# Optimization experiments

Hardware: AMD Instinct MI355X
Metric: run time of the kernel (lower is better)

The kernel has to match this reference:

```python
import jax, jax.numpy as jnp
import numpy as np

D_MODEL, D_STATE, D_CONV, EXPAND, N_HEADS = 768, 64, 4, 2, 12
D_INNER = D_MODEL * EXPAND           # 1536
HEAD_DIM = D_INNER // N_HEADS        # 128
IN_PROJ = D_INNER * 2 + N_HEADS * D_STATE * 2 + N_HEADS  # 4620
EPS = 1e-5


def setup_inputs() -> dict:
    key = jax.random.key(0)
    ks = jax.random.split(key, 8)
    s = lambda fan_in: 1.0 / np.sqrt(fan_in)
    return {
        "x": jax.random.normal(ks[0], (1, 1024, D_MODEL), dtype=jnp.float32),
        "W_in": jax.random.normal(ks[1], (IN_PROJ, D_MODEL), dtype=jnp.float32) * s(D_MODEL),
        "conv_w": jax.random.normal(ks[2], (D_INNER, D_CONV), dtype=jnp.float32) * s(D_CONV),
        "conv_b": jnp.zeros((D_INNER,), dtype=jnp.float32),
        "A_log": jnp.full((N_HEADS,), np.log(0.5), dtype=jnp.float32),
        "Dp": jnp.ones((N_HEADS,), dtype=jnp.float32),
        "dt_bias": jnp.zeros((N_HEADS,), dtype=jnp.float32),
        "W_out": jax.random.normal(ks[3], (D_MODEL, D_INNER), dtype=jnp.float32) * s(D_INNER),
        "norm_w": jnp.ones((D_INNER,), dtype=jnp.float32),
    }


def _causal_conv1d(x, w, b):
    # x: (B,L,Din), depthwise causal conv with kernel size D_CONV
    L = x.shape[1]
    xp = jnp.pad(x, ((0, 0), (D_CONV - 1, 0), (0, 0)))
    y = b
    for i in range(D_CONV):  # fixed small kernel, unrolled
        y = y + xp[:, i:i + L, :] * w[:, i]
    return y


def reference(x, W_in, conv_w, conv_b, A_log, Dp, dt_bias, W_out, norm_w):
    B_sz, L, _ = x.shape
    nh, ds, hd = N_HEADS, D_STATE, HEAD_DIM
    proj = jnp.einsum('bld,pd->blp', x, W_in)
    z = proj[:, :, :D_INNER]
    x_ssm = proj[:, :, D_INNER:2 * D_INNER]
    o = 2 * D_INNER
    Bm = proj[:, :, o:o + nh * ds].reshape(B_sz, L, nh, ds)
    Cm = proj[:, :, o + nh * ds:o + 2 * nh * ds].reshape(B_sz, L, nh, ds)
    dt_r = proj[:, :, o + 2 * nh * ds:]
    dt = jax.nn.softplus(dt_r) + dt_bias[None, None, :]          # (B,L,nh)

    x_ssm = jax.nn.silu(_causal_conv1d(x_ssm, conv_w, conv_b))
    x_ssm = x_ssm.reshape(B_sz, L, nh, hd)

    A = -jnp.exp(A_log)                                          # (nh,)
    log_decay = A[None, None, :] * dt                            # (B,L,nh)
    Phi = jnp.cumsum(log_decay, axis=1)
    dB = dt[..., None] * Bm                                      # (B,L,nh,ds)
    # b: (B,L,nh,hd,ds) outer product
    b = dB[:, :, :, None, :] * x_ssm[..., None]
    max_exp = 80.0
    exp_neg_Phi = jnp.exp(jnp.minimum(-Phi, max_exp))[..., None, None]
    b_cumsum = jnp.cumsum(exp_neg_Phi * b, axis=1)
    h = jnp.exp(Phi)[..., None, None] * b_cumsum                 # (B,L,nh,hd,ds)
    y = jnp.sum(Cm[:, :, :, None, :] * h, axis=-1)               # (B,L,nh,hd)
    y = y + Dp[None, None, :, None] * x_ssm
    y = y.reshape(B_sz, L, D_INNER)

    # RMSNorm then gate
    rms = jax.lax.rsqrt(jnp.mean(y * y, axis=-1, keepdims=True) + EPS)
    y = y * rms * norm_w
    y = y * jax.nn.silu(z)
    return jnp.einsum('bli,di->bld', y, W_out)
```

## Files before the change

kernel.cpp:

```cpp
#include <hip/hip_runtime.h>
#include <cmath>

#define LSEQ   1024
#define NPROJ  4620
#define NPADW  4736
#define DINNER 1536
#define NH     12
#define HDIM   128
#define OFF_Z  0
#define OFF_X  1536
#define OFF_B  3072
#define OFF_C  3840
#define OFF_DT 4608

typedef unsigned short u16;
typedef unsigned int u32;
typedef short bf16x8 __attribute__((ext_vector_type(8)));
typedef float f32x4 __attribute__((ext_vector_type(4)));

__device__ inline u16 f2b(float f) {
  unsigned u = __float_as_uint(f);
  return (u16)((u + 0x7fffu + ((u >> 16) & 1u)) >> 16);
}
__device__ inline float b2f(u16 h) { return __uint_as_float(((unsigned)h) << 16); }
__device__ inline u32 pk2(float a, float b) { return (u32)f2b(a) | ((u32)f2b(b) << 16); }

__device__ inline void gll16(const void* g, void* l) {
  __builtin_amdgcn_global_load_lds((const __attribute__((address_space(1))) void*)g,
                                   (__attribute__((address_space(3))) void*)l, 16, 0, 0);
}

#define S0N 196608
#define S1N 909312
#define S1V 887040
#define S2N 294912
__global__ __launch_bounds__(256) void ksplit_all(const float* __restrict__ x,
    const float* __restrict__ Wi, const float* __restrict__ Wo,
    u16* __restrict__ Ah, u16* __restrict__ Wh, u16* __restrict__ Woh) {
  int i = blockIdx.x * 256 + threadIdx.x;
  const float* src; u16* hi; int j, valid;
  if (i < S0N)            { src = x;  hi = Ah;  j = i;              valid = S0N; }
  else if (i < S0N + S1N) { src = Wi; hi = Wh;  j = i - S0N;        valid = S1V; }
  else                    { src = Wo; hi = Woh; j = i - S0N - S1N;  valid = S2N; }
  float4 v = (j < valid) ? ((const float4*)src)[j] : make_float4(0.f, 0.f, 0.f, 0.f);
  ((uint2*)hi)[j] = make_uint2(pk2(v.x, v.y), pk2(v.z, v.w));
}

template<int BM, int BN, int MAP, bool NG, bool OBF>
__global__ __launch_bounds__(256) void gemm1(const u16* __restrict__ Ah,
    const u16* __restrict__ Wh, void* __restrict__ Cv, float* __restrict__ dtr,
    int lda, int ldw, int Ksl, int Nreal, int ldc) {
  constexpr int PLA = BM * 64;
  constexpr int PB = PLA + BN * 64;
  constexpr int IA = BM / 8, ITOT = IA + BN / 8;
  constexpr int FRn = BN / 32;
  __shared__ u16 lds[2 * PB];
  const int tid = threadIdx.x;
  const int l = tid & 63, w = tid >> 6;
  const int wm = w >> 1, wn = w & 1;
  const int kg = l >> 4, li = l & 15;

  int b = blockIdx.x, m0, n0, koff, cslice = 0;
  if (MAP == 0) {
    int xcd = b & 7, idx = b >> 3;
    m0 = (idx & 15) * 64;
    n0 = (xcd * 5 + (idx >> 4)) * 128;
    koff = 0;
    if (NG && n0 >= NPADW) return;
  } else {
    int xcd = b & 7, idx = b >> 3;
    int gg = xcd * 6 + (idx >> 4);
    m0 = (idx & 15) * 64;
    n0 = (gg % 12) * 64;
    koff = (gg / 12) * 384;
    cslice = gg / 12;
  }

  const int srcg = ((l & 7) ^ (l >> 3)) * 8;
  auto stage = [&](int buf, int t) {
    const int k0 = koff + t * 64;
    for (int q = w; q < ITOT; q += 4) {
      const u16* gb; int r0b, ldk, dst;
      if (q < IA) { gb = Ah; r0b = m0 + 8 * q;        dst = 8 * q * 64;              ldk = lda; }
      else        { gb = Wh; r0b = n0 + 8 * (q - IA); dst = PLA + 8 * (q - IA) * 64; ldk = ldw; }
      gll16(gb + (size_t)(r0b + (l >> 3)) * ldk + k0 + srcg, &lds[buf * PB + dst]);
    }
  };
  auto rd = [&](int buf, int region, int row, int ks) -> bf16x8 {
    return *(const bf16x8*)&lds[buf * PB + region + row * 64 + (((ks * 4 + kg) ^ (row & 7)) << 3)];
  };

  f32x4 acc[2][FRn];
#pragma unroll
  for (int m = 0; m < 2; ++m)
#pragma unroll
    for (int n = 0; n < FRn; ++n) acc[m][n] = (f32x4){0.f, 0.f, 0.f, 0.f};

  const int NT = Ksl / 64;
  stage(0, 0);
  __syncthreads();
  int buf = 0;
  for (int t = 0; t < NT; ++t) {
    if (t + 1 < NT) stage(buf ^ 1, t + 1);
    bf16x8 af[2][2], wf[FRn][2];
#pragma unroll
    for (int ks = 0; ks < 2; ++ks) {
#pragma unroll
      for (int m = 0; m < 2; ++m)
        af[m][ks] = rd(buf, 0, wm * 32 + m * 16 + li, ks);
#pragma unroll
      for (int n = 0; n < FRn; ++n)
        wf[n][ks] = rd(buf, PLA, wn * (BN / 2) + n * 16 + li, ks);
    }
#pragma unroll
    for (int ks = 0; ks < 2; ++ks)
#pragma unroll
      for (int m = 0; m < 2; ++m)
#pragma unroll
        for (int n = 0; n < FRn; ++n)
          acc[m][n] = __builtin_amdgcn_mfma_f32_16x16x32_bf16(af[m][ks], wf[n][ks], acc[m][n], 0, 0, 0);
    __syncthreads();
    buf ^= 1;
  }
#pragma unroll
  for (int m = 0; m < 2; ++m) {
    int rbase = m0 + wm * 32 + m * 16 + kg * 4;
#pragma unroll
    for (int n = 0; n < FRn; ++n) {
      int col = n0 + wn * (BN / 2) + n * 16 + li;
      if (!NG || col < Nreal) {
#pragma unroll
        for (int r = 0; r < 4; ++r) {
          if (OBF) ((u16*)Cv)[(size_t)(rbase + r) * ldc + col] = f2b(acc[m][n][r]);
          else ((float*)Cv)[(size_t)(cslice * LSEQ + rbase + r) * ldc + col] = acc[m][n][r];
        }
        if (MAP == 0 && col >= OFF_DT) {
#pragma unroll
          for (int r = 0; r < 4; ++r)
            dtr[(size_t)(rbase + r) * NH + (col - OFF_DT)] = acc[m][n][r];
        }
      }
    }
  }
}

__global__ __launch_bounds__(256) void addk(const float* __restrict__ P,
    float* __restrict__ out) {
  const int S = LSEQ * 768 / 4;
  int i = blockIdx.x * 256 + threadIdx.x;
  float4 a = ((const float4*)P)[i];
  float4 b = ((const float4*)P)[i + S];
  float4 c = ((const float4*)P)[i + 2 * S];
  float4 d = ((const float4*)P)[i + 3 * S];
  ((float4*)out)[i] = make_float4(a.x + b.x + c.x + d.x, a.y + b.y + c.y + d.y,
                                  a.z + b.z + c.z + d.z, a.w + b.w + c.w + d.w);
}

__global__ __launch_bounds__(256) void dtphi(const float* __restrict__ dtraw,
    const float* __restrict__ A_log, const float* __restrict__ dt_bias,
    float* __restrict__ Phi, float* __restrict__ dts) {
  int h = blockIdx.x, tid = threadIdx.x;
  float Ac = -expf(A_log[h]);
  float bb = dt_bias[h];
  float v[4], s = 0.f;
#pragma unroll
  for (int u = 0; u < 4; ++u) {
    int t = tid * 4 + u;
    float xr = dtraw[(size_t)t * NH + h];
    float sp = (xr > 20.f) ? xr : log1pf(expf(xr));
    v[u] = sp + bb;
    s += v[u];
  }
  int lane = tid & 63, wv = tid >> 6;
  float ps = s;
#pragma unroll
  for (int d = 1; d < 64; d <<= 1) {
    float o = __shfl_up(ps, d);
    if (lane >= d) ps += o;
  }
  __shared__ float wsum[4];
  if (lane == 63) wsum[wv] = ps;
  __syncthreads();
  float off = 0.f;
  for (int w = 0; w < wv; ++w) off += wsum[w];
  float run = off + ps - s;
#pragma unroll
  for (int u = 0; u < 4; ++u) {
    int t = tid * 4 + u;
    run += v[u];
    Phi[t * NH + h] = Ac * run;
    dts[t * NH + h] = v[u];
  }
}

__global__ __launch_bounds__(256) void conv_state(const u16* __restrict__ proj,
    const float* __restrict__ cw, const float* __restrict__ cb,
    const float* __restrict__ Phi, const float* __restrict__ dts,
    u16* __restrict__ xactT, u16* __restrict__ Sloc) {
  const int k = blockIdx.x, h = blockIdx.y, tid = threadIdx.x;
  const int l = tid & 63, w = tid >> 6, kg = l >> 4, li = l & 15;
  __shared__ u16 Bw[4096];
  __shared__ u16 Xt[8192];
  __shared__ float wS[64];
  const int s0 = k * 64;
  if (tid < 64) {
    float pe = Phi[(s0 + 63) * NH + h];
    float p  = Phi[(s0 + tid) * NH + h];
    wS[tid] = expf(pe + fminf(-p, 80.f)) * dts[(s0 + tid) * NH + h];
  }
  __syncthreads();
#pragma unroll
  for (int u = 0; u < 2; ++u) {
    int idx = tid + u * 256;
    int s = idx >> 3, dq = (idx & 7) * 8;
    uint4 rw = *(const uint4*)(proj + (size_t)(s0 + s) * NPROJ + OFF_B + h * 64 + dq);
    float ws_ = wS[s];
    u32 pk[4] = {rw.x, rw.y, rw.z, rw.w};
#pragma unroll
    for (int j = 0; j < 8; ++j) {
      float bv = b2f((u16)(pk[j >> 1] >> ((j & 1) * 16)));
      int d = dq + j;
      Bw[d * 64 + (((s >> 3) ^ (d & 7)) << 3) + (s & 7)] = f2b(bv * ws_);
    }
  }
  {
    int c = tid & 127, th = tid >> 7;
    int cg = h * HDIM + c;
    float w0 = cw[cg * 4], w1 = cw[cg * 4 + 1], w2 = cw[cg * 4 + 2], w3 = cw[cg * 4 + 3];
    float bias = cb[cg];
    int tb = s0 + th * 32;
    auto P = [&](int t) { return (t >= 0) ? b2f(proj[(size_t)t * NPROJ + OFF_X + cg]) : 0.f; };
    float x0 = P(tb - 3), x1 = P(tb - 2), x2 = P(tb - 1);
    u32 pkb[16];
    float prev = 0.f;
#pragma unroll
    for (int i = 0; i < 32; ++i) {
      float x3 = P(tb + i);
      float a = bias;
      a = fmaf(x0, w0, a); a = fmaf(x1, w1, a); a = fmaf(x2, w2, a); a = fmaf(x3, w3, a);
      float sv = a / (1.f + expf(-a));
      if (i & 1) pkb[i >> 1] = pk2(prev, sv); else prev = sv;
      x0 = x1; x1 = x2; x2 = x3;
    }
#pragma unroll
    for (int g = 0; g < 4; ++g) {
      int sg = th * 4 + g;
      *(uint4*)&Xt[c * 64 + ((sg ^ (c & 7)) << 3)] =
          make_uint4(pkb[g * 4], pkb[g * 4 + 1], pkb[g * 4 + 2], pkb[g * 4 + 3]);
    }
    size_t xo = ((size_t)(k * NH + h) * 128 + c) * 64 + th * 32;
#pragma unroll
    for (int g = 0; g < 4; ++g)
      *(uint4*)(xactT + xo + g * 8) =
          make_uint4(pkb[g * 4], pkb[g * 4 + 1], pkb[g * 4 + 2], pkb[g * 4 + 3]);
  }
  __syncthreads();
  const int wm = w >> 1, wn = w & 1;
  auto rd = [&](const u16* reg, int row, int ks) -> bf16x8 {
    return *(const bf16x8*)&reg[row * 64 + (((ks * 4 + kg) ^ (row & 7)) << 3)];
  };
  f32x4 acc[4][2];
#pragma unroll
  for (int m = 0; m < 4; ++m)
#pragma unroll
    for (int n = 0; n < 2; ++n) acc[m][n] = (f32x4){0.f, 0.f, 0.f, 0.f};
#pragma unroll
  for (int ks = 0; ks < 2; ++ks) {
    bf16x8 xf[4], bf[2];
#pragma unroll
    for (int m = 0; m < 4; ++m) xf[m] = rd(Xt, wm * 64 + m * 16 + li, ks);
#pragma unroll
    for (int n = 0; n < 2; ++n) bf[n] = rd(Bw, wn * 32 + n * 16 + li, ks);
#pragma unroll
    for (int m = 0; m < 4; ++m)
#pragma unroll
      for (int n = 0; n < 2; ++n)
        acc[m][n] = __builtin_amdgcn_mfma_f32_16x16x32_bf16(xf[m], bf[n], acc[m][n], 0, 0, 0);
  }
  u16* dst = Sloc + (((size_t)(k * NH + h)) << 13);
#pragma unroll
  for (int m = 0; m < 4; ++m)
#pragma unroll
    for (int n = 0; n < 2; ++n)
#pragma unroll
      for (int r = 0; r < 4; ++r) {
        int c = wm * 64 + m * 16 + kg * 4 + r;
        int d = wn * 32 + n * 16 + li;
        dst[c * 64 + d] = f2b(acc[m][n][r]);
      }
}

__global__ __launch_bounds__(256) void ssm_out(const u16* __restrict__ proj,
    const u16* __restrict__ xactT, const float* __restrict__ Phi,
    const float* __restrict__ dts, const float* __restrict__ Dp,
    const u16* __restrict__ Sloc, u16* __restrict__ ybuf) {
  const int k = blockIdx.x, h = blockIdx.y, zh = blockIdx.z, tid = threadIdx.x;
  const int l = tid & 63, w = tid >> 6, kg = l >> 4, li = l & 15;
  const int wm = w >> 1, wn = w & 1;
  __shared__ u16 Cs[4096], Bs[4096], Ps[4096], Xs[4096], Ss[4096];
  __shared__ float phiT[64], eSs[64], dSs[64], eTs[64], wJ[16];
  const int t0 = k * 64;
  const int srcg = ((l & 7) ^ (l >> 3)) * 8;
  for (int q = w; q < 24; q += 4) {
    int rb = (q & 7) * 8;
    if (q < 8)
      gll16(proj + (size_t)(t0 + rb + (l >> 3)) * NPROJ + OFF_C + h * 64 + srcg, &Cs[rb * 64]);
    else if (q < 16)
      gll16(proj + (size_t)(t0 + rb + (l >> 3)) * NPROJ + OFF_B + h * 64 + srcg, &Bs[rb * 64]);
    else
      gll16(xactT + ((size_t)(k * NH + h) * 128 + zh * 64 + rb + (l >> 3)) * 64 + srcg, &Xs[rb * 64]);
  }
  if (tid < 64) {
    float p = Phi[(t0 + tid) * NH + h];
    phiT[tid] = p;
    eSs[tid] = fminf(-p, 80.f);
    dSs[tid] = dts[(t0 + tid) * NH + h];
    eTs[tid] = (k > 0) ? expf(p - Phi[(t0 - 1) * NH + h]) : 0.f;
  }
  if (tid < 16)
    wJ[tid] = (k > 0 && tid < k)
        ? expf(Phi[(k * 64 - 1) * NH + h] - Phi[(tid * 64 + 63) * NH + h]) : 0.f;
  __syncthreads();
  auto rd = [&](const u16* reg, int row, int ks) -> bf16x8 {
    return *(const bf16x8*)&reg[row * 64 + (((ks * 4 + kg) ^ (row & 7)) << 3)];
  };
  bf16x8 Cf[2][2];
  f32x4 accS[2][2];
#pragma unroll
  for (int m = 0; m < 2; ++m)
#pragma unroll
    for (int n = 0; n < 2; ++n) accS[m][n] = (f32x4){0.f, 0.f, 0.f, 0.f};
#pragma unroll
  for (int ks = 0; ks < 2; ++ks) {
    bf16x8 Bf[2];
#pragma unroll
    for (int m = 0; m < 2; ++m) Cf[m][ks] = rd(Cs, wm * 32 + m * 16 + li, ks);
#pragma unroll
    for (int n = 0; n < 2; ++n) Bf[n] = rd(Bs, wn * 32 + n * 16 + li, ks);
#pragma unroll
    for (int m = 0; m < 2; ++m)
#pragma unroll
      for (int n = 0; n < 2; ++n)
        accS[m][n] = __builtin_amdgcn_mfma_f32_16x16x32_bf16(Cf[m][ks], Bf[n], accS[m][n], 0, 0, 0);
  }
  if (k > 0) {
    float a16[16] = {};
    const int e0 = tid * 16;
    for (int j = 0; j < k; ++j) {
      const u16* sp = Sloc + (((size_t)(j * NH + h) * 128 + zh * 64) << 6) + e0;
      uint4 ra = *(const uint4*)sp;
      uint4 rb2 = *(const uint4*)(sp + 8);
      float wj = wJ[j];
      u32 pk[8] = {ra.x, ra.y, ra.z, ra.w, rb2.x, rb2.y, rb2.z, rb2.w};
#pragma unroll
      for (int i = 0; i < 16; ++i)
        a16[i] = fmaf(wj, b2f((u16)(pk[i >> 1] >> ((i & 1) * 16))), a16[i]);
    }
#pragma unroll
    for (int i = 0; i < 16; ++i) {
      int e = e0 + i, c = e >> 6, d = e & 63;
      Ss[c * 64 + (((d >> 3) ^ (c & 7)) << 3) + (d & 7)] = f2b(a16[i]);
    }
  }
#pragma unroll
  for (int m = 0; m < 2; ++m)
#pragma unroll
    for (int n = 0; n < 2; ++n)
#pragma unroll
      for (int r = 0; r < 4; ++r) {
        int t = wm * 32 + m * 16 + kg * 4 + r;
        int s = wn * 32 + n * 16 + li;
        float f = (s <= t) ? expf(phiT[t] + eSs[s]) * dSs[s] : 0.f;
        Ps[t * 64 + (((s >> 3) ^ (t & 7)) << 3) + (s & 7)] = f2b(accS[m][n][r] * f);
      }
  __syncthreads();
  f32x4 accY[2][2], acc2[2][2];
#pragma unroll
  for (int m = 0; m < 2; ++m)
#pragma unroll
    for (int n = 0; n < 2; ++n) {
      accY[m][n] = (f32x4){0.f, 0.f, 0.f, 0.f};
      acc2[m][n] = (f32x4){0.f, 0.f, 0.f, 0.f};
    }
#pragma unroll
  for (int ks = 0; ks < 2; ++ks) {
    bf16x8 Pf[2], Xf[2];
#pragma unroll
    for (int m = 0; m < 2; ++m) Pf[m] = rd(Ps, wm * 32 + m * 16 + li, ks);
#pragma unroll
    for (int n = 0; n < 2; ++n) Xf[n] = rd(Xs, wn * 32 + n * 16 + li, ks);
#pragma unroll
    for (int m = 0; m < 2; ++m)
#pragma unroll
      for (int n = 0; n < 2; ++n)
        accY[m][n] = __builtin_amdgcn_mfma_f32_16x16x32_bf16(Pf[m], Xf[n], accY[m][n], 0, 0, 0);
    if (k > 0) {
      bf16x8 Sf[2];
#pragma unroll
      for (int n = 0; n < 2; ++n) Sf[n] = rd(Ss, wn * 32 + n * 16 + li, ks);
#pragma unroll
      for (int m = 0; m < 2; ++m)
#pragma unroll
        for (int n = 0; n < 2; ++n)
          acc2[m][n] = __builtin_amdgcn_mfma_f32_16x16x32_bf16(Cf[m][ks], Sf[n], acc2[m][n], 0, 0, 0);
    }
  }
  float dp = Dp[h];
#pragma unroll
  for (int m = 0; m < 2; ++m)
#pragma unroll
    for (int n = 0; n < 2; ++n)
#pragma unroll
      for (int r = 0; r < 4; ++r) {
        int t = wm * 32 + m * 16 + kg * 4 + r;
        int c = wn * 32 + n * 16 + li;
        float xv = b2f(Xs[c * 64 + (((t >> 3) ^ (c & 7)) << 3) + (t & 7)]);
        float val = accY[m][n][r] + eTs[t] * acc2[m][n][r] + dp * xv;
        ybuf[(size_t)(t0 + t) * DINNER + h * HDIM + zh * 64 + c] = f2b(val);
      }
}

__global__ __launch_bounds__(256) void norm_gate(const u16* __restrict__ y,
    const u16* __restrict__ proj, const float* __restrict__ nw,
    u16* __restrict__ yh) {
  int t = blockIdx.x, tid = threadIdx.x;
  float v[6], ss = 0.f;
#pragma unroll
  for (int k = 0; k < 6; ++k) {
    v[k] = b2f(y[(size_t)t * DINNER + tid + k * 256]);
    ss = fmaf(v[k], v[k], ss);
  }
#pragma unroll
  for (int d = 1; d < 64; d <<= 1) ss += __shfl_xor(ss, d);
  __shared__ float wsum[4];
  int wv = tid >> 6;
  if ((tid & 63) == 0) wsum[wv] = ss;
  __syncthreads();
  float tot = wsum[0] + wsum[1] + wsum[2] + wsum[3];
  float rms = rsqrtf(tot / 1536.f + 1e-5f);
#pragma unroll
  for (int k = 0; k < 6; ++k) {
    int c = tid + k * 256;
    float z = b2f(proj[(size_t)t * NPROJ + OFF_Z + c]);
    float sz = z / (1.f + expf(-z));
    yh[(size_t)t * DINNER + c] = f2b(v[k] * rms * nw[c] * sz);
  }
}

extern "C" void kernel_launch(void* const* d_in, const int* in_sizes, int n_in,
                              void* d_out, int out_size, void* d_ws, size_t ws_size,
                              hipStream_t stream) {
  const float* x       = (const float*)d_in[0];
  const float* W_in    = (const float*)d_in[1];
  const float* conv_w  = (const float*)d_in[2];
  const float* conv_b  = (const float*)d_in[3];
  const float* A_log   = (const float*)d_in[4];
  const float* Dp      = (const float*)d_in[5];
  const float* dt_bias = (const float*)d_in[6];
  const float* W_out   = (const float*)d_in[7];
  const float* norm_w  = (const float*)d_in[8];
  float* out = (float*)d_out;

  char* base = (char*)d_ws;
  size_t o = 0;
  auto alloc = [&](size_t bytes) { char* r = base + o; o += (bytes + 255) & ~(size_t)255; return r; };
  u16*   proj  = (u16*)alloc((size_t)LSEQ * NPROJ * 2);
  float* dtraw = (float*)alloc((size_t)LSEQ * NH * 4);
  float* Phi   = (float*)alloc((size_t)LSEQ * NH * 4);
  float* dts   = (float*)alloc((size_t)LSEQ * NH * 4);
  u16*   Sloc  = (u16*)alloc((size_t)16 * NH * 8192 * 2);
  u16*   xactT = (u16*)alloc((size_t)16 * NH * 8192 * 2);
  u16*   ybuf  = (u16*)alloc((size_t)LSEQ * DINNER * 2);
  u16*   Ah    = (u16*)alloc((size_t)LSEQ * 768 * 2);
  u16*   Wh    = (u16*)alloc((size_t)NPADW * 768 * 2);
  u16*   Woh   = (u16*)alloc((size_t)768 * DINNER * 2);
  u16*   Yh    = (u16*)alloc((size_t)LSEQ * DINNER * 2);
  float* Pp    = (float*)alloc((size_t)4 * LSEQ * 768 * 4);

  ksplit_all<<<dim3((S0N + S1N + S2N) / 256), 256, 0, stream>>>(
      x, W_in, W_out, Ah, Wh, Woh);
  gemm1<64, 128, 0, true, true><<<dim3(640), 256, 0, stream>>>(
      Ah, Wh, proj, dtraw, 768, 768, 768, NPROJ, NPROJ);
  dtphi<<<dim3(NH), 256, 0, stream>>>(dtraw, A_log, dt_bias, Phi, dts);
  conv_state<<<dim3(16, NH), 256, 0, stream>>>(proj, conv_w, conv_b, Phi, dts, xactT, Sloc);
  ssm_out<<<dim3(16, NH, 2), 256, 0, stream>>>(proj, xactT, Phi, dts, Dp, Sloc, ybuf);
  norm_gate<<<dim3(LSEQ), 256, 0, stream>>>(ybuf, proj, norm_w, Yh);
  gemm1<64, 64, 1, false, false><<<dim3(768), 256, 0, stream>>>(
      Yh, Woh, Pp, nullptr, 1536, 1536, 384, 768, 768);
  addk<<<dim3(LSEQ * 768 / 4 / 256), 256, 0, stream>>>(Pp, out);
}
```

Measured before the change: 74.90 us.

## Add sequential chunk-state scan kernel and single-buffer GEMM LDS staging

Replaces the per-block O(k) weighted sum over all previous chunk states in ssm_out with a separate chunk_scan kernel that runs the inter-chunk recurrence once. Chunk states are now written in fp32 and converted to bf16 after the scan, and ssm_out loads the prefix state directly into LDS through the async-copy path. Separately, the GEMM drops LDS double buffering for a single buffer that waits on vmcnt and a barrier each iteration. That halves LDS use and may raise occupancy, but it gives up overlap of the global loads with the MFMA work. The scan adds one kernel launch and an extra fp32 round trip through memory.

Result: no change. 75.19 us (+0.4%).

```diff
diff --git a/kernel.cpp b/kernel.cpp
--- a/kernel.cpp
+++ b/kernel.cpp
@@ -51,10 +51,9 @@
     const u16* __restrict__ Wh, void* __restrict__ Cv, float* __restrict__ dtr,
     int lda, int ldw, int Ksl, int Nreal, int ldc) {
   constexpr int PLA = BM * 64;
-  constexpr int PB = PLA + BN * 64;
   constexpr int IA = BM / 8, ITOT = IA + BN / 8;
   constexpr int FRn = BN / 32;
-  __shared__ u16 lds[2 * PB];
+  __shared__ u16 lds[PLA + BN * 64];
   const int tid = threadIdx.x;
   const int l = tid & 63, w = tid >> 6;
   const int wm = w >> 1, wn = w & 1;
@@ -77,17 +76,17 @@
   }
 
   const int srcg = ((l & 7) ^ (l >> 3)) * 8;
-  auto stage = [&](int buf, int t) {
+  auto stage = [&](int t) {
     const int k0 = koff + t * 64;
     for (int q = w; q < ITOT; q += 4) {
       const u16* gb; int r0b, ldk, dst;
       if (q < IA) { gb = Ah; r0b = m0 + 8 * q;        dst = 8 * q * 64;              ldk = lda; }
       else        { gb = Wh; r0b = n0 + 8 * (q - IA); dst = PLA + 8 * (q - IA) * 64; ldk = ldw; }
-      gll16(gb + (size_t)(r0b + (l >> 3)) * ldk + k0 + srcg, &lds[buf * PB + dst]);
+      gll16(gb + (size_t)(r0b + (l >> 3)) * ldk + k0 + srcg, &lds[dst]);
     }
   };
-  auto rd = [&](int buf, int region, int row, int ks) -> bf16x8 {
-    return *(const bf16x8*)&lds[buf * PB + region + row * 64 + (((ks * 4 + kg) ^ (row & 7)) << 3)];
+  auto rd = [&](int region, int row, int ks) -> bf16x8 {
+    return *(const bf16x8*)&lds[region + row * 64 + (((ks * 4 + kg) ^ (row & 7)) << 3)];
   };
 
   f32x4 acc[2][FRn];
@@ -97,21 +96,22 @@
     for (int n = 0; n < FRn; ++n) acc[m][n] = (f32x4){0.f, 0.f, 0.f, 0.f};
 
   const int NT = Ksl / 64;
-  stage(0, 0);
-  __syncthreads();
-  int buf = 0;
+  stage(0);
+  asm volatile("s_waitcnt vmcnt(0)" ::: "memory");
+  __syncthreads();
   for (int t = 0; t < NT; ++t) {
-    if (t + 1 < NT) stage(buf ^ 1, t + 1);
     bf16x8 af[2][2], wf[FRn][2];
 #pragma unroll
     for (int ks = 0; ks < 2; ++ks) {
 #pragma unroll
       for (int m = 0; m < 2; ++m)
-        af[m][ks] = rd(buf, 0, wm * 32 + m * 16 + li, ks);
+        af[m][ks] = rd(0, wm * 32 + m * 16 + li, ks);
 #pragma unroll
       for (int n = 0; n < FRn; ++n)
-        wf[n][ks] = rd(buf, PLA, wn * (BN / 2) + n * 16 + li, ks);
-    }
+        wf[n][ks] = rd(PLA, wn * (BN / 2) + n * 16 + li, ks);
+    }
+    __syncthreads();
+    if (t + 1 < NT) stage(t + 1);
 #pragma unroll
     for (int ks = 0; ks < 2; ++ks)
 #pragma unroll
@@ -119,8 +119,10 @@
 #pragma unroll
         for (int n = 0; n < FRn; ++n)
           acc[m][n] = __builtin_amdgcn_mfma_f32_16x16x32_bf16(af[m][ks], wf[n][ks], acc[m][n], 0, 0, 0);
-    __syncthreads();
-    buf ^= 1;
+    if (t + 1 < NT) {
+      asm volatile("s_waitcnt vmcnt(0)" ::: "memory");
+      __syncthreads();
+    }
   }
 #pragma unroll
   for (int m = 0; m < 2; ++m) {
@@ -196,7 +198,7 @@
 __global__ __launch_bounds__(256) void conv_state(const u16* __restrict__ proj,
     const float* __restrict__ cw, const float* __restrict__ cb,
     const float* __restrict__ Phi, const float* __restrict__ dts,
-    u16* __restrict__ xactT, u16* __restrict__ Sloc) {
+    u16* __restrict__ xactT, float* __restrict__ SlocF) {
   const int k = blockIdx.x, h = blockIdx.y, tid = threadIdx.x;
   const int l = tid & 63, w = tid >> 6, kg = l >> 4, li = l & 15;
   __shared__ u16 Bw[4096];
@@ -277,7 +279,7 @@
       for (int n = 0; n < 2; ++n)
         acc[m][n] = __builtin_amdgcn_mfma_f32_16x16x32_bf16(xf[m], bf[n], acc[m][n], 0, 0, 0);
   }
-  u16* dst = Sloc + (((size_t)(k * NH + h)) << 13);
+  float* dst = SlocF + (((size_t)(k * NH + h)) << 13);
 #pragma unroll
   for (int m = 0; m < 4; ++m)
 #pragma unroll
@@ -286,29 +288,52 @@
       for (int r = 0; r < 4; ++r) {
         int c = wm * 64 + m * 16 + kg * 4 + r;
         int d = wn * 32 + n * 16 + li;
-        dst[c * 64 + d] = f2b(acc[m][n][r]);
+        dst[c * 64 + d] = acc[m][n][r];
       }
+}
+
+__global__ __launch_bounds__(256) void chunk_scan(const float* __restrict__ SlocF,
+    u16* __restrict__ SlocT, const float* __restrict__ Phi) {
+  int b = blockIdx.x;
+  int h = b >> 5;
+  int e = (b & 31) * 256 + threadIdx.x;
+  float run = SlocF[((size_t)h << 13) + e];
+  SlocT[((size_t)h << 13) + e] = f2b(run);
+#pragma unroll
+  for (int k = 1; k < 16; ++k) {
+    float lam = expf(Phi[(k * 64 + 63) * NH + h] - Phi[(k * 64 - 1) * NH + h]);
+    size_t o = ((size_t)(k * NH + h) << 13) + e;
+    run = fmaf(lam, run, SlocF[o]);
+    SlocT[o] = f2b(run);
+  }
 }
 
 __global__ __launch_bounds__(256) void ssm_out(const u16* __restrict__ proj,
     const u16* __restrict__ xactT, const float* __restrict__ Phi,
     const float* __restrict__ dts, const float* __restrict__ Dp,
-    const u16* __restrict__ Sloc, u16* __restrict__ ybuf) {
+    const u16* __restrict__ SlocT, u16* __restrict__ ybuf) {
   const int k = blockIdx.x, h = blockIdx.y, zh = blockIdx.z, tid = threadIdx.x;
   const int l = tid & 63, w = tid >> 6, kg = l >> 4, li = l & 15;
   const int wm = w >> 1, wn = w & 1;
   __shared__ u16 Cs[4096], Bs[4096], Ps[4096], Xs[4096], Ss[4096];
-  __shared__ float phiT[64], eSs[64], dSs[64], eTs[64], wJ[16];
+  __shared__ float phiT[64], eSs[64], dSs[64], eTs[64];
   const int t0 = k * 64;
   const int srcg = ((l & 7) ^ (l >> 3)) * 8;
-  for (int q = w; q < 24; q += 4) {
-    int rb = (q & 7) * 8;
-    if (q < 8)
-      gll16(proj + (size_t)(t0 + rb + (l >> 3)) * NPROJ + OFF_C + h * 64 + srcg, &Cs[rb * 64]);
-    else if (q < 16)
-      gll16(proj + (size_t)(t0 + rb + (l >> 3)) * NPROJ + OFF_B + h * 64 + srcg, &Bs[rb * 64]);
-    else
-      gll16(xactT + ((size_t)(k * NH + h) * 128 + zh * 64 + rb + (l >> 3)) * 64 + srcg, &Xs[rb * 64]);
+  {
+    const int qmax = (k > 0) ? 32 : 24;
+    const u16* ssrc = (k > 0)
+        ? SlocT + (((size_t)((k - 1) * NH + h) * 128 + zh * 64)) * 64 : nullptr;
+    for (int q = w; q < qmax; q += 4) {
+      int rb = (q & 7) * 8;
+      if (q < 8)
+        gll16(proj + (size_t)(t0 + rb + (l >> 3)) * NPROJ + OFF_C + h * 64 + srcg, &Cs[rb * 64]);
+      else if (q < 16)
+        gll16(proj + (size_t)(t0 + rb + (l >> 3)) * NPROJ + OFF_B + h * 64 + srcg, &Bs[rb * 64]);
+      else if (q < 24)
+        gll16(xactT + ((size_t)(k * NH + h) * 128 + zh * 64 + rb + (l >> 3)) * 64 + srcg, &Xs[rb * 64]);
+      else
+        gll16(ssrc + (size_t)(rb + (l >> 3)) * 64 + srcg, &Ss[rb * 64]);
+    }
   }
   if (tid < 64) {
     float p = Phi[(t0 + tid) * NH + h];
@@ -317,9 +342,6 @@
     dSs[tid] = dts[(t0 + tid) * NH + h];
     eTs[tid] = (k > 0) ? expf(p - Phi[(t0 - 1) * NH + h]) : 0.f;
   }
-  if (tid < 16)
-    wJ[tid] = (k > 0 && tid < k)
-        ? expf(Phi[(k * 64 - 1) * NH + h] - Phi[(tid * 64 + 63) * NH + h]) : 0.f;
   __syncthreads();
   auto rd = [&](const u16* reg, int row, int ks) -> bf16x8 {
     return *(const bf16x8*)&reg[row * 64 + (((ks * 4 + kg) ^ (row & 7)) << 3)];
@@ -342,25 +364,6 @@
 #pragma unroll
       for (int n = 0; n < 2; ++n)
         accS[m][n] = __builtin_amdgcn_mfma_f32_16x16x32_bf16(Cf[m][ks], Bf[n], accS[m][n], 0, 0, 0);
-  }
-  if (k > 0) {
-    float a16[16] = {};
-    const int e0 = tid * 16;
-    for (int j = 0; j < k; ++j) {
-      const u16* sp = Sloc + (((size_t)(j * NH + h) * 128 + zh * 64) << 6) + e0;
-      uint4 ra = *(const uint4*)sp;
-      uint4 rb2 = *(const uint4*)(sp + 8);
-      float wj = wJ[j];
-      u32 pk[8] = {ra.x, ra.y, ra.z, ra.w, rb2.x, rb2.y, rb2.z, rb2.w};
-#pragma unroll
-      for (int i = 0; i < 16; ++i)
-        a16[i] = fmaf(wj, b2f((u16)(pk[i >> 1] >> ((i & 1) * 16))), a16[i]);
-    }
-#pragma unroll
-    for (int i = 0; i < 16; ++i) {
-      int e = e0 + i, c = e >> 6, d = e & 63;
-      Ss[c * 64 + (((d >> 3) ^ (c & 7)) << 3) + (d & 7)] = f2b(a16[i]);
-    }
   }
 #pragma unroll
   for (int m = 0; m < 2; ++m)
@@ -468,7 +471,8 @@
   float* dtraw = (float*)alloc((size_t)LSEQ * NH * 4);
   float* Phi   = (float*)alloc((size_t)LSEQ * NH * 4);
   float* dts   = (float*)alloc((size_t)LSEQ * NH * 4);
-  u16*   Sloc  = (u16*)alloc((size_t)16 * NH * 8192 * 2);
+  float* SlocF = (float*)alloc((size_t)16 * NH * 8192 * 4);
+  u16*   SlocT = (u16*)alloc((size_t)16 * NH * 8192 * 2);
   u16*   xactT = (u16*)alloc((size_t)16 * NH * 8192 * 2);
   u16*   ybuf  = (u16*)alloc((size_t)LSEQ * DINNER * 2);
   u16*   Ah    = (u16*)alloc((size_t)LSEQ * 768 * 2);
@@ -482,8 +486,9 @@
   gemm1<64, 128, 0, true, true><<<dim3(640), 256, 0, stream>>>(
       Ah, Wh, proj, dtraw, 768, 768, 768, NPROJ, NPROJ);
   dtphi<<<dim3(NH), 256, 0, stream>>>(dtraw, A_log, dt_bias, Phi, dts);
-  conv_state<<<dim3(16, NH), 256, 0, stream>>>(proj, conv_w, conv_b, Phi, dts, xactT, Sloc);
-  ssm_out<<<dim3(16, NH, 2), 256, 0, stream>>>(proj, xactT, Phi, dts, Dp, Sloc, ybuf);
+  conv_state<<<dim3(16, NH), 256, 0, stream>>>(proj, conv_w, conv_b, Phi, dts, xactT, SlocF);
+  chunk_scan<<<dim3(NH * 32), 256, 0, stream>>>(SlocF, SlocT, Phi);
+  ssm_out<<<dim3(16, NH, 2), 256, 0, stream>>>(proj, xactT, Phi, dts, Dp, SlocT, ybuf);
   norm_gate<<<dim3(LSEQ), 256, 0, stream>>>(ybuf, proj, norm_w, Yh);
   gemm1<64, 64, 1, false, false><<<dim3(768), 256, 0, stream>>>(
       Yh, Woh, Pp, nullptr, 1536, 1536, 384, 768, 768);
```
